# Performance work log

Hardware: AMD Instinct MI355X
Metric: run time of the kernel (lower is better)

## Reference

```python
import jax, jax.numpy as jnp
import numpy as np

N_NODES = 1_000_000
N_EDGES = 16_000_000
RATIO = 0.5


def setup_inputs() -> dict:
    key = jax.random.key(0)
    k1, k2, k3 = jax.random.split(key, 3)
    x = jax.random.normal(k1, (N_NODES, 3), dtype=jnp.float32)
    edge_index = jax.random.randint(k2, (2, N_EDGES), 0, N_NODES, dtype=jnp.int32)
    weight = jax.random.normal(k3, (3,), dtype=jnp.float32)
    return {"x": x, "edge_index": edge_index, "weight": weight}


def reference(x, edge_index, weight):
    # PyG TopKPooling with in_channels=3, ratio=0.5, nonlinearity=tanh, min_score=None
    n = x.shape[0]
    k = int(np.ceil(RATIO * n))
    # per-node score: tanh( (x . w) / ||w|| )
    score = jnp.tanh((x @ weight) / jnp.linalg.norm(weight))  # [N]
    top_scores, perm = jax.lax.top_k(score, k)                # [k], [k]
    # gate selected node features by their score
    x_out = x[perm] * top_scores[:, None]                     # [k, 3]
    # relabel nodes: old index -> new index (or -1 if dropped)
    new_idx = jnp.full((n,), -1, dtype=edge_index.dtype)
    new_idx = new_idx.at[perm].set(jnp.arange(k, dtype=edge_index.dtype))
    new_edges = new_idx[edge_index]                           # [2, E]
    edge_mask = (new_edges[0] >= 0) & (new_edges[1] >= 0)     # [E]
    # jit-friendly fixed-shape output: invalid edges marked -1 + boolean mask
    new_edges = jnp.where(edge_mask[None, :], new_edges, -1)
    return x_out, new_edges, edge_mask
```

## Files before the change

### kernel.cpp

```cpp
#include <hip/hip_runtime.h>


#define N_NODES 1000000
#define N_EDGES 16000000
#define K_SEL   500000

typedef int      v4i __attribute__((ext_vector_type(4)));
typedef float    v4f __attribute__((ext_vector_type(4)));
typedef unsigned v4u __attribute__((ext_vector_type(4)));
typedef unsigned long long u64;

static constexpr int NDIG     = 256;
static constexpr int STHREADS = 256;
static constexpr int SIPT     = 8;
static constexpr int SCHUNK   = STHREADS * SIPT;
static constexpr int NB       = (N_NODES + SCHUNK - 1) / SCHUNK;
static constexpr int NWAVE    = STHREADS / 64;

static constexpr int EB_THREADS = 1024;
static constexpr int EB_EDGES   = EB_THREADS * 8;
static constexpr int NODE_SPLIT = 524288;
static constexpr int BM_WORDS   = (N_NODES + 31) / 32;
static constexpr int BM_W0      = NODE_SPLIT / 32;
static constexpr int BM_W1      = BM_WORDS - BM_W0;
static constexpr int BM_ALLOC   = 31264;

__device__ __forceinline__ float tanh_xla(float x) {
  const float kCutoff = 0.0004f;
  const float kClamp  = 7.90531110763549805f;
  float ax = fabsf(x);
  float xc = fminf(fmaxf(x, -kClamp), kClamp);
  float x2 = __fmul_rn(xc, xc);
  float p = -2.76076847742355e-16f;
  p = __fadd_rn(__fmul_rn(p, x2),  2.00018790482477e-13f);
  p = __fadd_rn(__fmul_rn(p, x2), -8.60467152213735e-11f);
  p = __fadd_rn(__fmul_rn(p, x2),  5.12229709037114e-08f);
  p = __fadd_rn(__fmul_rn(p, x2),  1.48572235717979e-05f);
  p = __fadd_rn(__fmul_rn(p, x2),  6.37261928875436e-04f);
  p = __fadd_rn(__fmul_rn(p, x2),  4.89352455891786e-03f);
  float num = __fmul_rn(xc, p);
  float q = 1.19825839466702e-06f;
  q = __fadd_rn(__fmul_rn(q, x2), 1.18534705686654e-04f);
  q = __fadd_rn(__fmul_rn(q, x2), 2.26843463243900e-03f);
  q = __fadd_rn(__fmul_rn(q, x2), 4.89352518554385e-03f);
  float r = __fdiv_rn(num, q);
  return (ax < kCutoff) ? x : r;
}

__global__ __launch_bounds__(256) void zero_meta(v4u* __restrict__ p, int n4) {
  int i = blockIdx.x * 256 + threadIdx.x;
  if (i < n4) p[i] = v4u{0u, 0u, 0u, 0u};
}

__global__ __launch_bounds__(STHREADS) void score_pass(
    const float* __restrict__ x, const float* __restrict__ w,
    u64* __restrict__ kp0, unsigned* __restrict__ histDM0) {
  __shared__ unsigned h[NDIG];
  const int t = threadIdx.x, b = blockIdx.x;
  const int base = b * SCHUNK;
  h[t] = 0;
  __syncthreads();
  float w0 = w[0], w1 = w[1], w2 = w[2];
  float nrm = __fsqrt_rn(__fadd_rn(__fadd_rn(__fmul_rn(w0, w0), __fmul_rn(w1, w1)),
                                   __fmul_rn(w2, w2)));
#pragma unroll
  for (int s = 0; s < SIPT; ++s) {
    int i = base + s * STHREADS + t;
    if (i < N_NODES) {
      float dot = __fadd_rn(__fadd_rn(__fmul_rn(x[3*i+0], w0), __fmul_rn(x[3*i+1], w1)),
                            __fmul_rn(x[3*i+2], w2));
      float z = __fdiv_rn(dot, nrm);
      float sc = tanh_xla(z);
      unsigned u = __float_as_uint(sc);
      if (u == 0x80000000u) u = 0u;
      u = (u & 0x80000000u) ? ~u : (u | 0x80000000u);
      unsigned key = ~u;
      kp0[i] = ((u64)key << 32) | (unsigned)i;
      atomicAdd(&h[key & 255u], 1u);
    }
  }
  __syncthreads();
  histDM0[t * NB + b] = h[t];
}

__global__ void radix_hist(const u64* __restrict__ kp,
                           unsigned* __restrict__ histDM, int shift) {
  __shared__ unsigned h[NDIG];
  int t = threadIdx.x;
  h[t] = 0;
  __syncthreads();
  int base = blockIdx.x * SCHUNK;
#pragma unroll
  for (int it = 0; it < SCHUNK / 256; ++it) {
    int i = base + it * 256 + t;
    if (i < N_NODES) atomicAdd(&h[(unsigned)(kp[i] >> shift) & 255u], 1u);
  }
  __syncthreads();
  histDM[t * NB + blockIdx.x] = h[t];
}

__global__ void scan_rows(unsigned* __restrict__ histDM, unsigned* __restrict__ rowsum) {
  __shared__ unsigned lds[512];
  int d = blockIdx.x, t = threadIdx.x;
  unsigned v = (t < NB) ? histDM[d * NB + t] : 0u;
  lds[t] = v;
  __syncthreads();
#pragma unroll
  for (int off = 1; off < 512; off <<= 1) {
    unsigned add = (t >= off) ? lds[t - off] : 0u;
    __syncthreads();
    lds[t] += add;
    __syncthreads();
  }
  if (t < NB) histDM[d * NB + t] = lds[t] - v;
  if (t == 511) rowsum[d] = lds[511];
}

template <int PASS>
__global__ __launch_bounds__(STHREADS) void scatter_pass(
    const u64* __restrict__ kin, u64* __restrict__ kout,
    const unsigned* __restrict__ histDM, const unsigned* __restrict__ rowsum,
    const float* __restrict__ x, int* __restrict__ ni,
    unsigned* __restrict__ bm, float* __restrict__ xout) {
  constexpr bool FINAL = (PASS == 3);
  __shared__ unsigned short whist[SIPT][NWAVE][NDIG];
  __shared__ unsigned goff[NDIG];
  __shared__ unsigned bexcl[NDIG];
  __shared__ unsigned scanbuf[NDIG];
  __shared__ u64 lkp[FINAL ? 1 : SCHUNK];
  const int t = threadIdx.x, b = blockIdx.x;
  const int wave = t >> 6, lane = t & 63;
  const int base = b * SCHUNK;
  const int sh = 32 + 8 * PASS;

  for (int j = t; j < SIPT * NWAVE * NDIG; j += STHREADS)
    ((unsigned short*)whist)[j] = 0;
  unsigned rs = rowsum[t];
  scanbuf[t] = rs;
  __syncthreads();
#pragma unroll
  for (int o = 1; o < NDIG; o <<= 1) {
    unsigned add = (t >= o) ? scanbuf[t - o] : 0u;
    __syncthreads();
    scanbuf[t] += add;
    __syncthreads();
  }
  goff[t] = (scanbuf[t] - rs) + histDM[t * NB + b];
  __syncthreads();

  u64 k[SIPT];
  unsigned dg[SIPT], lr[SIPT];
  bool val[SIPT];
#pragma unroll
  for (int s = 0; s < SIPT; ++s) {
    int i = base + s * STHREADS + t;
    val[s] = (i < N_NODES);
    k[s] = val[s] ? kin[i] : 0ull;
    dg[s] = (unsigned)(k[s] >> sh) & 255u;
  }
#pragma unroll
  for (int s = 0; s < SIPT; ++s) {
    unsigned long long m = ~0ull;
#pragma unroll
    for (int bb = 0; bb < 8; ++bb) {
      unsigned long long vote = __ballot((dg[s] >> bb) & 1u);
      m &= ((dg[s] >> bb) & 1u) ? vote : ~vote;
    }
    m &= __ballot(val[s]);
    lr[s] = (unsigned)__popcll(m & ((1ull << lane) - 1ull));
    if (val[s] && lr[s] == 0)
      whist[s][wave][dg[s]] = (unsigned short)__popcll(m);
  }
  __syncthreads();
  unsigned run = 0;
#pragma unroll
  for (int s = 0; s < SIPT; ++s)
#pragma unroll
    for (int wv = 0; wv < NWAVE; ++wv) {
      unsigned c = whist[s][wv][t];
      whist[s][wv][t] = (unsigned short)run;
      run += c;
    }
  scanbuf[t] = run;
  __syncthreads();
#pragma unroll
  for (int o = 1; o < NDIG; o <<= 1) {
    unsigned add = (t >= o) ? scanbuf[t - o] : 0u;
    __syncthreads();
    scanbuf[t] += add;
    __syncthreads();
  }
  bexcl[t] = scanbuf[t] - run;
  __syncthreads();

  if constexpr (!FINAL) {
#pragma unroll
    for (int s = 0; s < SIPT; ++s)
      if (val[s]) {
        unsigned lp = bexcl[dg[s]] + (unsigned)whist[s][wave][dg[s]] + lr[s];
        lkp[lp] = k[s];
      }
    __syncthreads();
    int nvalid = min(N_NODES - base, SCHUNK);
#pragma unroll
    for (int s = 0; s < SIPT; ++s) {
      int j = s * STHREADS + t;
      if (j < nvalid) {
        u64 kk = lkp[j];
        unsigned d = (unsigned)(kk >> sh) & 255u;
        kout[goff[d] + ((unsigned)j - bexcl[d])] = kk;
      }
    }
  } else {
#pragma unroll
    for (int s = 0; s < SIPT; ++s) {
      if (val[s]) {
        unsigned gpos = goff[dg[s]] + (unsigned)whist[s][wave][dg[s]] + lr[s];
        if (gpos < K_SEL) {
          int idx = (int)(unsigned)(k[s] & 0xFFFFFFFFull);
          ni[idx] = (int)gpos;
          atomicOr(&bm[idx >> 5], 1u << (idx & 31));
          unsigned uo = ~(unsigned)(k[s] >> 32);
          unsigned bits = (uo & 0x80000000u) ? (uo ^ 0x80000000u) : ~uo;
          float sc = __uint_as_float(bits);
          xout[3*gpos+0] = __fmul_rn(x[3*idx+0], sc);
          xout[3*gpos+1] = __fmul_rn(x[3*idx+1], sc);
          xout[3*gpos+2] = __fmul_rn(x[3*idx+2], sc);
        }
      }
    }
  }
}

__global__ __launch_bounds__(EB_THREADS) void edge_kernel(
    const int* __restrict__ ei, const int* __restrict__ ni,
    const unsigned* __restrict__ bm,
    float* __restrict__ oedge, float* __restrict__ omask) {
  __shared__ unsigned lbm[BM_W0];
  int t = threadIdx.x;
  long long e = (long long)blockIdx.x * EB_EDGES + (long long)t * 8;
  bool act = (e + 8 <= (long long)N_EDGES);

  v4i a0{}, a1{}, b0{}, b1{};
  if (act) {
    a0 = __builtin_nontemporal_load((const v4i*)(ei + e));
    a1 = __builtin_nontemporal_load((const v4i*)(ei + e) + 1);
    b0 = __builtin_nontemporal_load((const v4i*)(ei + (long long)N_EDGES + e));
    b1 = __builtin_nontemporal_load((const v4i*)(ei + (long long)N_EDGES + e) + 1);
  }
  int A[8], B[8];
#pragma unroll
  for (int j = 0; j < 4; ++j) {
    A[j] = a0[j]; A[4 + j] = a1[j];
    B[j] = b0[j]; B[4 + j] = b1[j];
  }
#pragma unroll
  for (int j = 0; j < BM_W0 / (EB_THREADS * 4); ++j)
    ((v4u*)lbm)[t + j * EB_THREADS] = ((const v4u*)bm)[t + j * EB_THREADS];
  __syncthreads();
  unsigned bA = 0, bB = 0;
  if (act) {
#pragma unroll
    for (int j = 0; j < 8; ++j) {
      if (A[j] < NODE_SPLIT) bA |= ((lbm[A[j] >> 5] >> (A[j] & 31)) & 1u) << j;
      if (B[j] < NODE_SPLIT) bB |= ((lbm[B[j] >> 5] >> (B[j] & 31)) & 1u) << j;
    }
  }
  __syncthreads();
  {
    const v4u* src = (const v4u*)(bm + BM_W0);
    for (int j = t; j < (BM_W1 + 3) / 4; j += EB_THREADS)
      ((v4u*)lbm)[j] = src[j];
  }
  __syncthreads();
  if (act) {
#pragma unroll
    for (int j = 0; j < 8; ++j) {
      if (A[j] >= NODE_SPLIT) {
        int q = A[j] - NODE_SPLIT;
        bA |= ((lbm[q >> 5] >> (q & 31)) & 1u) << j;
      }
      if (B[j] >= NODE_SPLIT) {
        int q = B[j] - NODE_SPLIT;
        bB |= ((lbm[q >> 5] >> (q & 31)) & 1u) << j;
      }
    }
    unsigned mm = bA & bB;
    float fa[8], fb[8], fm[8];
#pragma unroll
    for (int j = 0; j < 8; ++j) {
      bool m = (mm >> j) & 1u;
      int na = -1, nb = -1;
      if (m) { na = ni[A[j]]; nb = ni[B[j]]; }
      fa[j] = m ? (float)na : -1.0f;
      fb[j] = m ? (float)nb : -1.0f;
      fm[j] = m ? 1.0f : 0.0f;
    }
    __builtin_nontemporal_store(*(const v4f*)&fa[0], (v4f*)(oedge + e));
    __builtin_nontemporal_store(*(const v4f*)&fa[4], (v4f*)(oedge + e) + 1);
    __builtin_nontemporal_store(*(const v4f*)&fb[0], (v4f*)(oedge + (long long)N_EDGES + e));
    __builtin_nontemporal_store(*(const v4f*)&fb[4], (v4f*)(oedge + (long long)N_EDGES + e) + 1);
    __builtin_nontemporal_store(*(const v4f*)&fm[0], (v4f*)(omask + e));
    __builtin_nontemporal_store(*(const v4f*)&fm[4], (v4f*)(omask + e) + 1);
  }
}

extern "C" void kernel_launch(void* const* d_in, const int* in_sizes, int n_in,
                              void* d_out, int out_size, void* d_ws, size_t ws_size,
                              hipStream_t stream) {
  const float* x  = (const float*)d_in[0];
  const int*   ei = (const int*)d_in[1];
  const float* w  = (const float*)d_in[2];
  float* out = (float*)d_out;

  char* ws = (char*)d_ws;
  size_t off = 0;
  auto alloc = [&](size_t bytes) -> void* {
    void* ptr = ws + off;
    off += (bytes + 255) & ~size_t(255);
    return ptr;
  };
  u64*      kp0    = (u64*)alloc((size_t)N_NODES * 8);
  u64*      kp1    = (u64*)alloc((size_t)N_NODES * 8);
  int*      ni     = (int*)alloc((size_t)N_NODES * 4);
  unsigned* rowsum = (unsigned*)alloc((size_t)NDIG * 4);
  unsigned* histDM0= (unsigned*)alloc((size_t)NDIG * NB * 4);
  unsigned* histDM1= (unsigned*)alloc((size_t)NDIG * NB * 4);
  unsigned* histDM2= (unsigned*)alloc((size_t)NDIG * NB * 4);
  unsigned* histDM3= (unsigned*)alloc((size_t)NDIG * NB * 4);
  unsigned* bm     = (unsigned*)alloc((size_t)BM_ALLOC * 4);
  (void)ws_size; (void)in_sizes; (void)n_in; (void)out_size;

  zero_meta <<<(BM_ALLOC / 4 + 255) / 256, 256, 0, stream>>>((v4u*)bm, BM_ALLOC / 4);
  score_pass<<<NB, STHREADS, 0, stream>>>(x, w, kp0, histDM0);

  scan_rows<<<NDIG, 512, 0, stream>>>(histDM0, rowsum);
  scatter_pass<0><<<NB, STHREADS, 0, stream>>>(kp0, kp1, histDM0, rowsum,
                                               nullptr, nullptr, nullptr, nullptr);
  radix_hist<<<NB, 256, 0, stream>>>(kp1, histDM1, 40);
  scan_rows<<<NDIG, 512, 0, stream>>>(histDM1, rowsum);
  scatter_pass<1><<<NB, STHREADS, 0, stream>>>(kp1, kp0, histDM1, rowsum,
                                               nullptr, nullptr, nullptr, nullptr);
  radix_hist<<<NB, 256, 0, stream>>>(kp0, histDM2, 48);
  scan_rows<<<NDIG, 512, 0, stream>>>(histDM2, rowsum);
  scatter_pass<2><<<NB, STHREADS, 0, stream>>>(kp0, kp1, histDM2, rowsum,
                                               nullptr, nullptr, nullptr, nullptr);
  radix_hist<<<NB, 256, 0, stream>>>(kp1, histDM3, 56);
  scan_rows<<<NDIG, 512, 0, stream>>>(histDM3, rowsum);
  scatter_pass<3><<<NB, STHREADS, 0, stream>>>(kp1, nullptr, histDM3, rowsum,
                                               x, ni, bm, out);

  edge_kernel<<<(N_EDGES + EB_EDGES - 1) / EB_EDGES, EB_THREADS, 0, stream>>>(
      ei, ni, bm, out + 1500000, out + 33500000);
}
```

Baseline: 221.5 us.

## Fold digit-histogram scans into scatter passes and zero bitmap in score kernel

Removes the separate scan_rows kernels and the zero_meta kernel, cutting five launches. Each scatter block now reads the whole block-major histogram column for its digit, summing all blocks and the blocks before it to get its global offset, then does the 256-digit scan in LDS. Histograms are stored block-major so these reads coalesce across threads. The price is redundant work: every block reads about NB*256 counters, which is quadratic in block count.

```diff
diff --git a/kernel.cpp b/kernel.cpp
--- a/kernel.cpp
+++ b/kernel.cpp
@@ -47,18 +47,18 @@
   return (ax < kCutoff) ? x : r;
 }
 
-__global__ __launch_bounds__(256) void zero_meta(v4u* __restrict__ p, int n4) {
-  int i = blockIdx.x * 256 + threadIdx.x;
-  if (i < n4) p[i] = v4u{0u, 0u, 0u, 0u};
-}
-
 __global__ __launch_bounds__(STHREADS) void score_pass(
     const float* __restrict__ x, const float* __restrict__ w,
-    u64* __restrict__ kp0, unsigned* __restrict__ histDM0) {
+    u64* __restrict__ kp0, unsigned* __restrict__ histDM0,
+    unsigned* __restrict__ bm) {
   __shared__ unsigned h[NDIG];
   const int t = threadIdx.x, b = blockIdx.x;
   const int base = b * SCHUNK;
   h[t] = 0;
+  if (t < 64) {
+    int wi = b * 64 + t;
+    if (wi < BM_ALLOC) bm[wi] = 0u;
+  }
   __syncthreads();
   float w0 = w[0], w1 = w[1], w2 = w[2];
   float nrm = __fsqrt_rn(__fadd_rn(__fadd_rn(__fmul_rn(w0, w0), __fmul_rn(w1, w1)),
@@ -80,7 +80,7 @@
     }
   }
   __syncthreads();
-  histDM0[t * NB + b] = h[t];
+  histDM0[b * NDIG + t] = h[t];
 }
 
 __global__ void radix_hist(const u64* __restrict__ kp,
@@ -96,30 +96,13 @@
     if (i < N_NODES) atomicAdd(&h[(unsigned)(kp[i] >> shift) & 255u], 1u);
   }
   __syncthreads();
-  histDM[t * NB + blockIdx.x] = h[t];
-}
-
-__global__ void scan_rows(unsigned* __restrict__ histDM, unsigned* __restrict__ rowsum) {
-  __shared__ unsigned lds[512];
-  int d = blockIdx.x, t = threadIdx.x;
-  unsigned v = (t < NB) ? histDM[d * NB + t] : 0u;
-  lds[t] = v;
-  __syncthreads();
-#pragma unroll
-  for (int off = 1; off < 512; off <<= 1) {
-    unsigned add = (t >= off) ? lds[t - off] : 0u;
-    __syncthreads();
-    lds[t] += add;
-    __syncthreads();
-  }
-  if (t < NB) histDM[d * NB + t] = lds[t] - v;
-  if (t == 511) rowsum[d] = lds[511];
+  histDM[blockIdx.x * NDIG + t] = h[t];
 }
 
 template <int PASS>
 __global__ __launch_bounds__(STHREADS) void scatter_pass(
     const u64* __restrict__ kin, u64* __restrict__ kout,
-    const unsigned* __restrict__ histDM, const unsigned* __restrict__ rowsum,
+    const unsigned* __restrict__ histDM,
     const float* __restrict__ x, int* __restrict__ ni,
     unsigned* __restrict__ bm, float* __restrict__ xout) {
   constexpr bool FINAL = (PASS == 3);
@@ -135,18 +118,6 @@
 
   for (int j = t; j < SIPT * NWAVE * NDIG; j += STHREADS)
     ((unsigned short*)whist)[j] = 0;
-  unsigned rs = rowsum[t];
-  scanbuf[t] = rs;
-  __syncthreads();
-#pragma unroll
-  for (int o = 1; o < NDIG; o <<= 1) {
-    unsigned add = (t >= o) ? scanbuf[t - o] : 0u;
-    __syncthreads();
-    scanbuf[t] += add;
-    __syncthreads();
-  }
-  goff[t] = (scanbuf[t] - rs) + histDM[t * NB + b];
-  __syncthreads();
 
   u64 k[SIPT];
   unsigned dg[SIPT], lr[SIPT];
@@ -156,8 +127,43 @@
     int i = base + s * STHREADS + t;
     val[s] = (i < N_NODES);
     k[s] = val[s] ? kin[i] : 0ull;
+  }
+
+  unsigned sum_all = 0, sum_below = 0;
+  {
+    int j = 0;
+    for (; j + 4 <= NB; j += 4) {
+      unsigned c0 = histDM[(j + 0) * NDIG + t];
+      unsigned c1 = histDM[(j + 1) * NDIG + t];
+      unsigned c2 = histDM[(j + 2) * NDIG + t];
+      unsigned c3 = histDM[(j + 3) * NDIG + t];
+      sum_all += c0 + c1 + c2 + c3;
+      if (j + 0 < b) sum_below += c0;
+      if (j + 1 < b) sum_below += c1;
+      if (j + 2 < b) sum_below += c2;
+      if (j + 3 < b) sum_below += c3;
+    }
+    for (; j < NB; ++j) {
+      unsigned c = histDM[j * NDIG + t];
+      sum_all += c;
+      if (j < b) sum_below += c;
+    }
+  }
+  scanbuf[t] = sum_all;
+  __syncthreads();
+#pragma unroll
+  for (int o = 1; o < NDIG; o <<= 1) {
+    unsigned add = (t >= o) ? scanbuf[t - o] : 0u;
+    __syncthreads();
+    scanbuf[t] += add;
+    __syncthreads();
+  }
+  goff[t] = (scanbuf[t] - sum_all) + sum_below;
+  __syncthreads();
+
+#pragma unroll
+  for (int s = 0; s < SIPT; ++s)
     dg[s] = (unsigned)(k[s] >> sh) & 255u;
-  }
 #pragma unroll
   for (int s = 0; s < SIPT; ++s) {
     unsigned long long m = ~0ull;
@@ -323,7 +329,6 @@
   u64*      kp0    = (u64*)alloc((size_t)N_NODES * 8);
   u64*      kp1    = (u64*)alloc((size_t)N_NODES * 8);
   int*      ni     = (int*)alloc((size_t)N_NODES * 4);
-  unsigned* rowsum = (unsigned*)alloc((size_t)NDIG * 4);
   unsigned* histDM0= (unsigned*)alloc((size_t)NDIG * NB * 4);
   unsigned* histDM1= (unsigned*)alloc((size_t)NDIG * NB * 4);
   unsigned* histDM2= (unsigned*)alloc((size_t)NDIG * NB * 4);
@@ -331,23 +336,17 @@
   unsigned* bm     = (unsigned*)alloc((size_t)BM_ALLOC * 4);
   (void)ws_size; (void)in_sizes; (void)n_in; (void)out_size;
 
-  zero_meta <<<(BM_ALLOC / 4 + 255) / 256, 256, 0, stream>>>((v4u*)bm, BM_ALLOC / 4);
-  score_pass<<<NB, STHREADS, 0, stream>>>(x, w, kp0, histDM0);
-
-  scan_rows<<<NDIG, 512, 0, stream>>>(histDM0, rowsum);
-  scatter_pass<0><<<NB, STHREADS, 0, stream>>>(kp0, kp1, histDM0, rowsum,
+  score_pass<<<NB, STHREADS, 0, stream>>>(x, w, kp0, histDM0, bm);
+  scatter_pass<0><<<NB, STHREADS, 0, stream>>>(kp0, kp1, histDM0,
                                                nullptr, nullptr, nullptr, nullptr);
   radix_hist<<<NB, 256, 0, stream>>>(kp1, histDM1, 40);
-  scan_rows<<<NDIG, 512, 0, stream>>>(histDM1, rowsum);
-  scatter_pass<1><<<NB, STHREADS, 0, stream>>>(kp1, kp0, histDM1, rowsum,
+  scatter_pass<1><<<NB, STHREADS, 0, stream>>>(kp1, kp0, histDM1,
                                                nullptr, nullptr, nullptr, nullptr);
   radix_hist<<<NB, 256, 0, stream>>>(kp0, histDM2, 48);
-  scan_rows<<<NDIG, 512, 0, stream>>>(histDM2, rowsum);
-  scatter_pass<2><<<NB, STHREADS, 0, stream>>>(kp0, kp1, histDM2, rowsum,
+  scatter_pass<2><<<NB, STHREADS, 0, stream>>>(kp0, kp1, histDM2,
                                                nullptr, nullptr, nullptr, nullptr);
   radix_hist<<<NB, 256, 0, stream>>>(kp1, histDM3, 56);
-  scan_rows<<<NDIG, 512, 0, stream>>>(histDM3, rowsum);
-  scatter_pass<3><<<NB, STHREADS, 0, stream>>>(kp1, nullptr, histDM3, rowsum,
+  scatter_pass<3><<<NB, STHREADS, 0, stream>>>(kp1, nullptr, histDM3,
                                                x, ni, bm, out);
 
   edge_kernel<<<(N_EDGES + EB_EDGES - 1) / EB_EDGES, EB_THREADS, 0, stream>>>(
```

Measured after the change: 290.3 us. 31.0% more time.
